# Optimization experiments

Hardware: AMD Instinct MI355X
Metric: run time of the kernel (lower is better)

Reference implementation:

```python
import jax, jax.numpy as jnp
import numpy as np

B, NPG, DEG = 512, 128, 16          # graphs, nodes/graph, out-degree
N = B * NPG                          # 65536 nodes
E = N * DEG                          # 1048576 edges
IN_DIM, HID, HEADS = 11, 32, 4
K1 = int(np.ceil(0.8 * NPG))         # 103 nodes/graph after pool1
K2 = int(np.ceil(0.8 * K1))          # 83 nodes/graph after pool2


def gat_conv(x, src, dst, mask, W, a_s, a_d, b, n_nodes):
    # PyG GATConv (concat=True, add_self_loops=True, eval mode -> no dropout)
    xp = (x @ W).reshape(n_nodes, HEADS, HID)            # [N,H,C]
    as_ = jnp.einsum('nhc,hc->nh', xp, a_s)
    ad_ = jnp.einsum('nhc,hc->nh', xp, a_d)
    loop = jnp.arange(n_nodes)
    s = jnp.concatenate([src, loop])
    d = jnp.concatenate([dst, loop])
    m = jnp.concatenate([mask, jnp.ones(n_nodes, bool)])
    logit = jax.nn.leaky_relu(as_[s] + ad_[d], 0.2)      # [E+N,H]
    logit = jnp.where(m[:, None], logit, -1e9)
    mx = jax.ops.segment_max(logit, d, num_segments=n_nodes)
    ex = jnp.exp(logit - mx[d]) * m[:, None]
    den = jax.ops.segment_sum(ex, d, num_segments=n_nodes)
    alpha = ex / (den[d] + 1e-16)                        # segment softmax over dst
    out = jax.ops.segment_sum(alpha[:, :, None] * xp[s], d, num_segments=n_nodes)
    return out.reshape(n_nodes, HEADS * HID) + b


def topk_pool(x, src, dst, mask, w, npg, k):
    # PyG TopKPooling: score = tanh((x*w).sum(-1)/||w||); keep top ceil(ratio*n) per graph
    nb = x.shape[0] // npg
    score = jnp.tanh((x @ w) / jnp.linalg.norm(w))
    vals, idx = jax.lax.top_k(score.reshape(nb, npg), k)  # [B,k]
    perm = (idx + (jnp.arange(nb) * npg)[:, None]).reshape(-1)
    x_new = x[perm] * vals.reshape(-1, 1)
    remap = jnp.full(nb * npg, -1).at[perm].set(jnp.arange(nb * k))
    ns, nd = remap[src], remap[dst]
    m = mask & (ns >= 0) & (nd >= 0)
    return x_new, jnp.where(m, ns, 0), jnp.where(m, nd, 0), m


def setup_inputs():
    key = jax.random.key(0)
    ks = jax.random.split(key, 24)
    s = 0.05
    x = jax.random.normal(ks[0], (N, IN_DIM), jnp.float32)
    src = jnp.repeat(jnp.arange(N), DEG)
    dst = (src // NPG) * NPG + jax.random.randint(ks[1], (E,), 0, NPG)
    edge_index = jnp.stack([src, dst])
    edge_attr = jax.random.normal(ks[2], (E, 4), jnp.float32)
    batch = jnp.repeat(jnp.arange(B), NPG)
    p = dict(
        W_g1=jax.random.normal(ks[3], (IN_DIM, HEADS * HID), jnp.float32) * s,
        att_src1=jax.random.normal(ks[4], (HEADS, HID), jnp.float32) * s,
        att_dst1=jax.random.normal(ks[5], (HEADS, HID), jnp.float32) * s,
        b_g1=jnp.zeros((HEADS * HID,), jnp.float32),
        W_t1=jax.random.normal(ks[6], (HEADS * HID, HID), jnp.float32) * s,
        b_t1=jnp.zeros((HID,), jnp.float32),
        pool_w1=jax.random.normal(ks[7], (HID,), jnp.float32) * s,
        W_g2=jax.random.normal(ks[8], (HID, HEADS * HID), jnp.float32) * s,
        att_src2=jax.random.normal(ks[9], (HEADS, HID), jnp.float32) * s,
        att_dst2=jax.random.normal(ks[10], (HEADS, HID), jnp.float32) * s,
        b_g2=jnp.zeros((HEADS * HID,), jnp.float32),
        W_t2=jax.random.normal(ks[11], (HEADS * HID, HID), jnp.float32) * s,
        b_t2=jnp.zeros((HID,), jnp.float32),
        pool_w2=jax.random.normal(ks[12], (HID,), jnp.float32) * s,
        W_l1=jax.random.normal(ks[13], (2 * HID, 256), jnp.float32) * s,
        b_l1=jnp.zeros((256,), jnp.float32),
        W_l2=jax.random.normal(ks[14], (256, 1024), jnp.float32) * s,
        b_l2=jnp.zeros((1024,), jnp.float32),
        W_l3=jax.random.normal(ks[15], (1024, 1), jnp.float32) * s,
        b_l3=jnp.zeros((1,), jnp.float32),
    )
    return dict(x=x, edge_index=edge_index, edge_attr=edge_attr, batch=batch, **p)


def reference(x, edge_index, edge_attr, batch,
              W_g1, att_src1, att_dst1, b_g1, W_t1, b_t1, pool_w1,
              W_g2, att_src2, att_dst2, b_g2, W_t2, b_t2, pool_w2,
              W_l1, b_l1, W_l2, b_l2, W_l3, b_l3):
    # edge_attr is ignored (GATConv built without edge_dim); batch is implicit
    # in the fixed equal-size graph layout.  Eval mode -> dropout disabled.
    src, dst = edge_index[0], edge_index[1]
    mask = jnp.ones(E, bool)
    h = jax.nn.relu(gat_conv(x, src, dst, mask, W_g1, att_src1, att_dst1, b_g1, N))
    h = h @ W_t1 + b_t1
    h, src, dst, mask = topk_pool(h, src, dst, mask, pool_w1, NPG, K1)
    h1 = h.reshape(B, K1, HID)
    g1 = jnp.concatenate([h1.max(1), h1.mean(1)], axis=1)   # [B, 2*HID]
    h = jax.nn.relu(gat_conv(h, src, dst, mask, W_g2, att_src2, att_dst2, b_g2, B * K1))
    h = h @ W_t2 + b_t2
    h, src, dst, mask = topk_pool(h, src, dst, mask, pool_w2, K1, K2)
    h2 = h.reshape(B, K2, HID)
    g2 = jnp.concatenate([h2.max(1), h2.mean(1)], axis=1)
    g = g1 + g2
    g = jax.nn.relu(g @ W_l1 + b_l1)
    g = jax.nn.relu(g @ W_l2 + b_l2)
    return g @ W_l3 + b_l3                                   # [B,1]
```

## Files before the change

kernel.cpp:

```cpp
#include <hip/hip_runtime.h>
#include <math.h>

constexpr int NPGc  = 128;
constexpr int NG    = 512;
constexpr int EPGc  = 2048;
constexpr int ETOT  = 1048576;
constexpr int IND   = 11;
constexpr int HIDc  = 32;
constexpr int FD    = 128;
constexpr int K1c   = 103;
constexpr int K2c   = 83;
constexpr int NN    = NG * NPGc;
constexpr int N2c   = NG * K1c;

__device__ __forceinline__ float lrelu(float x){ return fmaxf(x, 0.2f*x); }

template<int KIN>
__device__ void foldDev(const float* __restrict__ Wg, const float* __restrict__ avs,
                        const float* __restrict__ avd, float* __restrict__ S, float* __restrict__ D, int t)
{
    if (t < KIN * 4) {
        int k = t >> 2, h = t & 3;
        float s = 0.f, d = 0.f;
        for (int j = 0; j < HIDc; j++) {
            float w = Wg[k*FD + h*HIDc + j];
            s = fmaf(w, avs[h*HIDc + j], s);
            d = fmaf(w, avd[h*HIDc + j], d);
        }
        S[t] = s; D[t] = d;
    }
}
__global__ void k_fold2(const float* W1, const float* s1, const float* d1, float* S1, float* D1,
                        const float* W2, const float* s2, const float* d2, float* S2, float* D2)
{
    if (blockIdx.x == 0) foldDev<IND>(W1, s1, d1, S1, D1, threadIdx.x);
    else                 foldDev<HIDc>(W2, s2, d2, S2, D2, threadIdx.x);
}

template<bool REMAP>
__global__ __launch_bounds__(256) void k_csr(const int* __restrict__ ei, const int* __restrict__ rankv,
                                             int* __restrict__ csrOff, unsigned char* __restrict__ csrSB,
                                             int nnode)
{
    int g = blockIdx.x, t = threadIdx.x;
    __shared__ int cnt[128], cur[128], offL[129];
    __shared__ unsigned char sbL[EPGc];
    __shared__ signed char rmap[NPGc];
    if (t < 128) cnt[t] = 0;
    if constexpr (REMAP) { if (t < NPGc) rmap[t] = (signed char)rankv[g*NPGc + t]; }
    __syncthreads();
    const int* dstG = ei + ETOT + g * EPGc;
    int sn[8], dn[8];
    #pragma unroll
    for (int q = 0; q < 8; q++) {
        int e = t + 256*q;
        int dO = dstG[e] - g * NPGc, s0 = e >> 4;
        if constexpr (REMAP) {
            int s = rmap[s0], d = rmap[dO];
            bool ok = (s >= 0 && d >= 0);
            sn[q] = s; dn[q] = ok ? d : -1;
        } else { sn[q] = s0; dn[q] = dO; }
        if (dn[q] >= 0) atomicAdd(&cnt[dn[q]], 1);
    }
    __syncthreads();
    if (t < 64) {
        int c0 = cnt[2*t], c1 = cnt[2*t + 1], ps = c0 + c1, P = ps;
        #pragma unroll
        for (int dlt = 1; dlt < 64; dlt <<= 1) { int v = __shfl_up(P, dlt); if (t >= dlt) P += v; }
        int E0 = P - ps;
        offL[2*t] = E0; offL[2*t + 1] = E0 + c0;
        cur[2*t] = E0; cur[2*t + 1] = E0 + c0;
        if (t == 63) offL[128] = P;
    }
    __syncthreads();
    #pragma unroll
    for (int q = 0; q < 8; q++) {
        if (dn[q] >= 0) { int pos = atomicAdd(&cur[dn[q]], 1); sbL[pos] = (unsigned char)sn[q]; }
    }
    __syncthreads();
    if (t < 128) ((int4*)(csrSB + (size_t)g * EPGc))[t] = ((const int4*)sbL)[t];
    if (t <= nnode) csrOff[g*132 + t] = offL[t];
}

template<int NNODE, int KIN>
__global__ __launch_bounds__(256) void k_gat(
    const float* __restrict__ xin, const float* __restrict__ Wg,
    const float* __restrict__ WsS, const float* __restrict__ WsD,
    const int* __restrict__ csrOff, const unsigned char* __restrict__ csrSB,
    const float* __restrict__ bias, float* __restrict__ outp)
{
    int g = blockIdx.x, h = blockIdx.y, t = threadIdx.x;
    constexpr int UN = (NNODE*KIN > EPGc ? NNODE*KIN : EPGc);
    __shared__ __align__(16) float xpL[NNODE * 36];
    __shared__ __align__(16) float uni[UN];
    __shared__ __align__(16) unsigned char sbL[EPGc];
    __shared__ float asL[NNODE], adL[NNODE], mM[NNODE], sfW[NNODE], sDen[NNODE];
    __shared__ int offL[NNODE + 1];
    __shared__ float WL[KIN * 32];
    __shared__ float WsSL[KIN], WsDL[KIN], bL[32];

    float* xF  = uni;
    float* wEL = uni;

    {
        const float* xg = xin + (size_t)g * NNODE * KIN;
        if constexpr ((KIN & 3) == 0) {
            for (int i = t; i < NNODE * (KIN/4); i += 256)
                ((float4*)xF)[i] = ((const float4*)xg)[i];
        } else {
            for (int i = t; i < NNODE * KIN; i += 256) xF[i] = xg[i];
        }
    }
    for (int i = t; i < KIN * 32; i += 256) { int k = i >> 5, c = i & 31; WL[i] = Wg[k*FD + h*32 + c]; }
    if (t < KIN) { WsSL[t] = WsS[t*4 + h]; WsDL[t] = WsD[t*4 + h]; }
    if (t < 32) bL[t] = bias[h*32 + t];
    if (t <= NNODE) offL[t] = csrOff[g*132 + t];
    if (t < 128) ((int4*)sbL)[t] = ((const int4*)(csrSB + (size_t)g * EPGc))[t];
    __syncthreads();

    for (int p = t; p < NNODE * 32; p += 256) {
        int n = p >> 5, c = p & 31;
        const float* xr = xF + n * KIN;
        float acc = 0.f;
        #pragma unroll
        for (int k = 0; k < KIN; k++) acc = fmaf(xr[k], WL[k*32 + c], acc);
        xpL[n*36 + c] = acc;
    }
    if (t < NNODE) {
        const float* xr = xF + t * KIN;
        float s = 0.f, d = 0.f;
        #pragma unroll
        for (int k = 0; k < KIN; k++) { float v = xr[k]; s = fmaf(v, WsSL[k], s); d = fmaf(v, WsDL[k], d); }
        asL[t] = s; adL[t] = d;
    }
    __syncthreads();

    if (t < NNODE) {
        float as_n = asL[t], adn = adL[t];
        int lo = offL[t], hi = offL[t + 1];
        float mx = as_n;
        for (int i = lo; i < hi; i++) mx = fmaxf(mx, asL[sbL[i]]);
        float m = lrelu(mx + adn);
        float ws = expf(lrelu(as_n + adn) - m);
        float den = ws;
        for (int i = lo; i < hi; i++) {
            float w = expf(lrelu(asL[sbL[i]] + adn) - m);
            wEL[i] = w; den += w;
        }
        mM[t] = m; sfW[t] = ws; sDen[t] = den;
    }
    __syncthreads();

    const float4* X4 = (const float4*)xpL;
    for (int p = t; p < NNODE * 8; p += 256) {
        int n = p >> 3, c4 = p & 7;
        float w0 = sfW[n];
        float4 v = X4[n*9 + c4];
        float4 acc; acc.x = w0*v.x; acc.y = w0*v.y; acc.z = w0*v.z; acc.w = w0*v.w;
        int lo = offL[n], hi = offL[n + 1];
        for (int i = lo; i < hi; i++) {
            int sc = sbL[i]; float w = wEL[i];
            float4 u = X4[sc*9 + c4];
            acc.x = fmaf(w, u.x, acc.x); acc.y = fmaf(w, u.y, acc.y);
            acc.z = fmaf(w, u.z, acc.z); acc.w = fmaf(w, u.w, acc.w);
        }
        float inv = 1.f / (sDen[n] + 1e-16f);
        float4 r;
        r.x = fmaxf(fmaf(acc.x, inv, bL[c4*4 + 0]), 0.f);
        r.y = fmaxf(fmaf(acc.y, inv, bL[c4*4 + 1]), 0.f);
        r.z = fmaxf(fmaf(acc.z, inv, bL[c4*4 + 2]), 0.f);
        r.w = fmaxf(fmaf(acc.w, inv, bL[c4*4 + 3]), 0.f);
        *(float4*)(outp + (size_t)(g * NNODE + n) * FD + h*32 + c4*4) = r;
    }
}

__global__ __launch_bounds__(256) void k_lin(const float* __restrict__ in,
    const float* __restrict__ W, const float* __restrict__ b, float* __restrict__ outp)
{
    __shared__ float WtL[FD * HIDc];
    int t = threadIdx.x;
    for (int i = t; i < FD * HIDc / 4; i += 256) ((float4*)WtL)[i] = ((const float4*)W)[i];
    __syncthreads();
    int j = t & 31, rg = t >> 5;
    int r0 = blockIdx.x * 32 + rg * 4;
    const float* i0 = in + (size_t)r0 * FD;
    float bj = b[j];
    float a0 = bj, a1 = bj, a2 = bj, a3 = bj;
    for (int k4 = 0; k4 < 32; k4++) {
        float4 v0 = *(const float4*)(i0 + k4*4);
        float4 v1 = *(const float4*)(i0 + FD + k4*4);
        float4 v2 = *(const float4*)(i0 + 2*FD + k4*4);
        float4 v3 = *(const float4*)(i0 + 3*FD + k4*4);
        float w0 = WtL[(k4*4 + 0)*HIDc + j], w1 = WtL[(k4*4 + 1)*HIDc + j];
        float w2 = WtL[(k4*4 + 2)*HIDc + j], w3 = WtL[(k4*4 + 3)*HIDc + j];
        a0 = fmaf(v0.x, w0, a0); a0 = fmaf(v0.y, w1, a0); a0 = fmaf(v0.z, w2, a0); a0 = fmaf(v0.w, w3, a0);
        a1 = fmaf(v1.x, w0, a1); a1 = fmaf(v1.y, w1, a1); a1 = fmaf(v1.z, w2, a1); a1 = fmaf(v1.w, w3, a1);
        a2 = fmaf(v2.x, w0, a2); a2 = fmaf(v2.y, w1, a2); a2 = fmaf(v2.z, w2, a2); a2 = fmaf(v2.w, w3, a2);
        a3 = fmaf(v3.x, w0, a3); a3 = fmaf(v3.y, w1, a3); a3 = fmaf(v3.z, w2, a3); a3 = fmaf(v3.w, w3, a3);
    }
    size_t ob = (size_t)r0 * HIDc + j;
    outp[ob] = a0; outp[ob + 32] = a1; outp[ob + 64] = a2; outp[ob + 96] = a3;
}

template<int NIN, int KEEP, bool FIRST>
__global__ __launch_bounds__(256) void k_pool(const float* __restrict__ ht,
    const float* __restrict__ pw, float* __restrict__ xnew, int* __restrict__ rankv,
    float* __restrict__ gfeat, const float* __restrict__ gprev)
{
    int g = blockIdx.x, t = threadIdx.x;
    __shared__ float htL[NIN * 33];
    __shared__ float scoreL[NIN], valL[NIN];
    __shared__ int rnkL[NIN];
    for (int i = t; i < NIN * 8; i += 256) {
        int n = i >> 3, q = i & 7;
        float4 v = *(const float4*)(ht + (size_t)(g*NIN + n)*HIDc + q*4);
        float* dst = htL + n*33 + q*4;
        dst[0] = v.x; dst[1] = v.y; dst[2] = v.z; dst[3] = v.w;
    }
    __syncthreads();
    float nrm; { float ss = 0.f; for (int k = 0; k < HIDc; k++) { float w = pw[k]; ss = fmaf(w, w, ss); } nrm = sqrtf(ss); }
    if (t < NIN) {
        float dot = 0.f;
        for (int k = 0; k < HIDc; k++) dot = fmaf(htL[t*33 + k], pw[k], dot);
        float val = tanhf(dot / nrm);
        scoreL[t] = val; valL[t] = val;
    }
    __syncthreads();
    if (t < NIN) {
        float si = scoreL[t]; int rank = 0;
        for (int q = 0; q < NIN; q++) {
            float sj = scoreL[q];
            rank += (sj > si || (sj == si && q < t)) ? 1 : 0;
        }
        rnkL[t] = (rank < KEEP) ? rank : -1;
        if (FIRST) rankv[g*NPGc + t] = rnkL[t];
    }
    __syncthreads();
    if (FIRST) {
        for (int p = t; p < NIN * 32; p += 256) {
            int n = p >> 5, jj = p & 31;
            int rk = rnkL[n];
            if (rk >= 0) xnew[((size_t)g*KEEP + rk)*HIDc + jj] = htL[n*33 + jj] * valL[n];
        }
    }
    if (t < HIDc) {
        float mx = -INFINITY, sm = 0.f;
        for (int n = 0; n < NIN; n++) {
            if (rnkL[n] >= 0) { float v = htL[n*33 + t] * valL[n]; mx = fmaxf(mx, v); sm += v; }
        }
        float mean = sm / (float)KEEP;
        if (FIRST) {
            gfeat[(size_t)g*64 + t]      = mx;
            gfeat[(size_t)g*64 + 32 + t] = mean;
        } else {
            gfeat[(size_t)g*64 + t]      = gprev[(size_t)g*64 + t] + mx;
            gfeat[(size_t)g*64 + 32 + t] = gprev[(size_t)g*64 + 32 + t] + mean;
        }
    }
}

__global__ __launch_bounds__(256) void k_mlpA(const float* __restrict__ gsum,
    const float* __restrict__ W1, const float* __restrict__ b1,
    const float* __restrict__ W2, const float* __restrict__ b2,
    const float* __restrict__ W3, float* __restrict__ part)
{
    int gb = blockIdx.x, q = blockIdx.y, t = threadIdx.x;
    int g0 = gb * 4;
    __shared__ float gL[256];
    __shared__ float h1L[1024];
    __shared__ float4 red[256];
    gL[t] = gsum[(size_t)g0*64 + t];
    __syncthreads();
    float bv = b1[t];
    float a0 = bv, a1 = bv, a2 = bv, a3 = bv;
    #pragma unroll 4
    for (int k = 0; k < 64; k++) {
        float w = W1[k*256 + t];
        a0 = fmaf(gL[k], w, a0); a1 = fmaf(gL[64 + k], w, a1);
        a2 = fmaf(gL[128 + k], w, a2); a3 = fmaf(gL[192 + k], w, a3);
    }
    h1L[t] = fmaxf(a0, 0.f); h1L[256 + t] = fmaxf(a1, 0.f);
    h1L[512 + t] = fmaxf(a2, 0.f); h1L[768 + t] = fmaxf(a3, 0.f);
    __syncthreads();
    int o = q * 256 + t;
    float b2v = b2[o], w3 = W3[o];
    float c0 = b2v, c1 = b2v, c2 = b2v, c3 = b2v;
    const float* w2c = W2 + o;
    #pragma unroll 8
    for (int i = 0; i < 256; i++) {
        float w = w2c[(size_t)i * 1024];
        c0 = fmaf(h1L[i], w, c0); c1 = fmaf(h1L[256 + i], w, c1);
        c2 = fmaf(h1L[512 + i], w, c2); c3 = fmaf(h1L[768 + i], w, c3);
    }
    red[t] = make_float4(fmaxf(c0, 0.f)*w3, fmaxf(c1, 0.f)*w3, fmaxf(c2, 0.f)*w3, fmaxf(c3, 0.f)*w3);
    __syncthreads();
    for (int s = 128; s > 0; s >>= 1) {
        if (t < s) { float4 a = red[t], b = red[t + s]; a.x += b.x; a.y += b.y; a.z += b.z; a.w += b.w; red[t] = a; }
        __syncthreads();
    }
    if (t == 0) {
        float4 r = red[0];
        part[(size_t)(g0 + 0)*4 + q] = r.x;
        part[(size_t)(g0 + 1)*4 + q] = r.y;
        part[(size_t)(g0 + 2)*4 + q] = r.z;
        part[(size_t)(g0 + 3)*4 + q] = r.w;
    }
}

__global__ void k_mlpB(const float* __restrict__ part, const float* __restrict__ b3,
                       float* __restrict__ outp)
{
    int g = blockIdx.x * 256 + threadIdx.x;
    if (g < NG) {
        float4 p = ((const float4*)part)[g];
        outp[g] = ((p.x + p.y) + (p.z + p.w)) + b3[0];
    }
}

extern "C" void kernel_launch(void* const* d_in, const int* in_sizes, int n_in,
                              void* d_out, int out_size, void* d_ws, size_t ws_size,
                              hipStream_t stream)
{
    const float* x    = (const float*)d_in[0];
    const int*   ei   = (const int*)  d_in[1];
    const float* W_g1 = (const float*)d_in[4];
    const float* as1w = (const float*)d_in[5];
    const float* ad1w = (const float*)d_in[6];
    const float* b_g1 = (const float*)d_in[7];
    const float* W_t1 = (const float*)d_in[8];
    const float* b_t1 = (const float*)d_in[9];
    const float* pw1  = (const float*)d_in[10];
    const float* W_g2 = (const float*)d_in[11];
    const float* as2w = (const float*)d_in[12];
    const float* ad2w = (const float*)d_in[13];
    const float* b_g2 = (const float*)d_in[14];
    const float* W_t2 = (const float*)d_in[15];
    const float* b_t2 = (const float*)d_in[16];
    const float* pw2  = (const float*)d_in[17];
    const float* W_l1 = (const float*)d_in[18];
    const float* b_l1 = (const float*)d_in[19];
    const float* W_l2 = (const float*)d_in[20];
    const float* b_l2 = (const float*)d_in[21];
    const float* W_l3 = (const float*)d_in[22];
    const float* b_l3 = (const float*)d_in[23];
    float* out = (float*)d_out;

    char* ws = (char*)d_ws;
    size_t off = 0;
    auto alloc = [&](size_t bytes) -> void* {
        void* p = (void*)(ws + off);
        off += ((bytes + 255) / 256) * 256;
        return p;
    };
    float* hg1   = (float*)alloc((size_t)NN * FD * 4);
    float* ht1   = (float*)alloc((size_t)NN * HIDc * 4);
    float* x2    = (float*)alloc((size_t)N2c * HIDc * 4);
    int*   rank1 = (int*)  alloc((size_t)NN * 4);
    float* g1    = (float*)alloc((size_t)NG * 64 * 4);
    float* gsum  = (float*)alloc((size_t)NG * 64 * 4);
    float* part  = (float*)alloc((size_t)NG * 4 * 4);
    float* wsS1  = (float*)alloc(64 * 4);
    float* wsD1  = (float*)alloc(64 * 4);
    float* wsS2  = (float*)alloc(128 * 4);
    float* wsD2  = (float*)alloc(128 * 4);
    int*   off1  = (int*)  alloc((size_t)NG * 132 * 4);
    unsigned char* sb1 = (unsigned char*)alloc((size_t)NG * EPGc);
    int*   off2  = (int*)  alloc((size_t)NG * 132 * 4);
    unsigned char* sb2 = (unsigned char*)alloc((size_t)NG * EPGc);
    float* hg2 = hg1;
    float* ht2 = ht1;

    k_fold2<<<2, 128, 0, stream>>>(W_g1, as1w, ad1w, wsS1, wsD1,
                                   W_g2, as2w, ad2w, wsS2, wsD2);
    k_csr<false><<<NG, 256, 0, stream>>>(ei, nullptr, off1, sb1, NPGc);

    k_gat<NPGc, IND><<<dim3(NG, 4), 256, 0, stream>>>(
        x, W_g1, wsS1, wsD1, off1, sb1, b_g1, hg1);
    k_lin<<<NN/32, 256, 0, stream>>>(hg1, W_t1, b_t1, ht1);
    k_pool<NPGc, K1c, true><<<NG, 256, 0, stream>>>(
        ht1, pw1, x2, rank1, g1, nullptr);

    k_csr<true><<<NG, 256, 0, stream>>>(ei, rank1, off2, sb2, K1c);
    k_gat<K1c, HIDc><<<dim3(NG, 4), 256, 0, stream>>>(
        x2, W_g2, wsS2, wsD2, off2, sb2, b_g2, hg2);
    k_lin<<<N2c/32, 256, 0, stream>>>(hg2, W_t2, b_t2, ht2);
    k_pool<K1c, K2c, false><<<NG, 256, 0, stream>>>(
        ht2, pw2, nullptr, nullptr, gsum, g1);

    k_mlpA<<<dim3(NG/4, 4), 256, 0, stream>>>(gsum, W_l1, b_l1, W_l2, b_l2, W_l3, part);
    k_mlpB<<<2, 256, 0, stream>>>(part, b_l3, out);
}
```

Measured before the change: 329.4 us.

## Fuse GAT, linear transform and top-k pool into one per-graph layer kernel

Replaces the separate GAT (one block per graph per head), linear and pooling kernels with one kernel per graph that loops over the four heads and accumulates the 128->32 linear projection in registers before pooling in shared memory. This removes the global round trips of the 128-wide GAT output and the 32-wide linear output, and two launches per layer. The softmax max and exp are now edge-parallel, using a float-flip atomicMax on a new per-edge destination array produced by the CSR kernel. The trade-offs are less block parallelism (512 blocks instead of 2048 for GAT), heavy shared memory use that limits occupancy, and the heads now running one after another inside a block.

```diff
diff --git a/kernel.cpp b/kernel.cpp
--- a/kernel.cpp
+++ b/kernel.cpp
@@ -15,6 +15,15 @@
 
 __device__ __forceinline__ float lrelu(float x){ return fmaxf(x, 0.2f*x); }
 
+__device__ __forceinline__ unsigned flipF(float f){
+    unsigned u = __float_as_uint(f);
+    return u ^ (unsigned)(((int)u >> 31) | 0x80000000);
+}
+__device__ __forceinline__ float unflipF(unsigned u){
+    unsigned m = ((u >> 31) - 1u) | 0x80000000u;
+    return __uint_as_float(u ^ m);
+}
+
 template<int KIN>
 __device__ void foldDev(const float* __restrict__ Wg, const float* __restrict__ avs,
                         const float* __restrict__ avd, float* __restrict__ S, float* __restrict__ D, int t)
@@ -40,11 +49,11 @@
 template<bool REMAP>
 __global__ __launch_bounds__(256) void k_csr(const int* __restrict__ ei, const int* __restrict__ rankv,
                                              int* __restrict__ csrOff, unsigned char* __restrict__ csrSB,
-                                             int nnode)
+                                             unsigned char* __restrict__ csrDB, int nnode)
 {
     int g = blockIdx.x, t = threadIdx.x;
     __shared__ int cnt[128], cur[128], offL[129];
-    __shared__ unsigned char sbL[EPGc];
+    __shared__ unsigned char sbL[EPGc], dbL[EPGc];
     __shared__ signed char rmap[NPGc];
     if (t < 128) cnt[t] = 0;
     if constexpr (REMAP) { if (t < NPGc) rmap[t] = (signed char)rankv[g*NPGc + t]; }
@@ -75,160 +84,217 @@
     __syncthreads();
     #pragma unroll
     for (int q = 0; q < 8; q++) {
-        if (dn[q] >= 0) { int pos = atomicAdd(&cur[dn[q]], 1); sbL[pos] = (unsigned char)sn[q]; }
-    }
-    __syncthreads();
-    if (t < 128) ((int4*)(csrSB + (size_t)g * EPGc))[t] = ((const int4*)sbL)[t];
+        if (dn[q] >= 0) {
+            int pos = atomicAdd(&cur[dn[q]], 1);
+            sbL[pos] = (unsigned char)sn[q];
+            dbL[pos] = (unsigned char)dn[q];
+        }
+    }
+    __syncthreads();
+    if (t < 128) {
+        ((int4*)(csrSB + (size_t)g * EPGc))[t] = ((const int4*)sbL)[t];
+        ((int4*)(csrDB + (size_t)g * EPGc))[t] = ((const int4*)dbL)[t];
+    }
     if (t <= nnode) csrOff[g*132 + t] = offL[t];
 }
 
-template<int NNODE, int KIN>
-__global__ __launch_bounds__(256) void k_gat(
+template<int NNODE, int KIN, int KEEP, bool FIRST>
+__global__ __launch_bounds__(256, 4) void k_layer(
     const float* __restrict__ xin, const float* __restrict__ Wg,
     const float* __restrict__ WsS, const float* __restrict__ WsD,
+    const float* __restrict__ bg,
+    const float* __restrict__ Wt, const float* __restrict__ bt,
+    const float* __restrict__ pw,
     const int* __restrict__ csrOff, const unsigned char* __restrict__ csrSB,
-    const float* __restrict__ bias, float* __restrict__ outp)
-{
-    int g = blockIdx.x, h = blockIdx.y, t = threadIdx.x;
-    constexpr int UN = (NNODE*KIN > EPGc ? NNODE*KIN : EPGc);
-    __shared__ __align__(16) float xpL[NNODE * 36];
-    __shared__ __align__(16) float uni[UN];
-    __shared__ __align__(16) unsigned char sbL[EPGc];
-    __shared__ float asL[NNODE], adL[NNODE], mM[NNODE], sfW[NNODE], sDen[NNODE];
+    const unsigned char* __restrict__ csrDB,
+    float* __restrict__ xnew, int* __restrict__ rankv,
+    float* __restrict__ gfeat, const float* __restrict__ gprev)
+{
+    constexpr int NP   = (NNODE + 3) & ~3;
+    constexpr int NGRP = NP / 4;
+    int g = blockIdx.x, t = threadIdx.x;
+
+    __shared__ __align__(16) float xFT[KIN * NP];
+    __shared__ __align__(16) float WfL[KIN * FD];
+    __shared__ __align__(16) float WtL[FD * HIDc];
+    __shared__ __align__(16) float xpL[NP * 36];
+    __shared__ float wEu[EPGc];
+    __shared__ unsigned char sbL[EPGc], dbL[EPGc];
     __shared__ int offL[NNODE + 1];
-    __shared__ float WL[KIN * 32];
-    __shared__ float WsSL[KIN], WsDL[KIN], bL[32];
-
-    float* xF  = uni;
-    float* wEL = uni;
+    __shared__ float asL[NNODE], adL[NNODE], sfW[NNODE], sDi[NNODE];
+    __shared__ unsigned maxU[NNODE];
+    __shared__ __align__(8) float admL[NNODE * 2];
+    __shared__ float WsSL[KIN * 4], WsDL[KIN * 4], bgL[FD], btL[HIDc];
 
     {
         const float* xg = xin + (size_t)g * NNODE * KIN;
-        if constexpr ((KIN & 3) == 0) {
-            for (int i = t; i < NNODE * (KIN/4); i += 256)
-                ((float4*)xF)[i] = ((const float4*)xg)[i];
-        } else {
-            for (int i = t; i < NNODE * KIN; i += 256) xF[i] = xg[i];
-        }
-    }
-    for (int i = t; i < KIN * 32; i += 256) { int k = i >> 5, c = i & 31; WL[i] = Wg[k*FD + h*32 + c]; }
-    if (t < KIN) { WsSL[t] = WsS[t*4 + h]; WsDL[t] = WsD[t*4 + h]; }
-    if (t < 32) bL[t] = bias[h*32 + t];
+        for (int i = t; i < NNODE * KIN; i += 256) {
+            int n = i / KIN, k = i - n * KIN;
+            xFT[k * NP + n] = xg[i];
+        }
+        if constexpr (NP > NNODE) {
+            for (int i = t; i < KIN * (NP - NNODE); i += 256) {
+                int k = i / (NP - NNODE), n = NNODE + (i % (NP - NNODE));
+                xFT[k * NP + n] = 0.f;
+            }
+        }
+    }
+    for (int i = t; i < KIN * FD / 4; i += 256) ((float4*)WfL)[i] = ((const float4*)Wg)[i];
+    for (int i = t; i < FD * HIDc / 4; i += 256) ((float4*)WtL)[i] = ((const float4*)Wt)[i];
+    for (int i = t; i < KIN * 4; i += 256) { WsSL[i] = WsS[i]; WsDL[i] = WsD[i]; }
+    if (t < FD) bgL[t] = bg[t];
+    if (t < HIDc) btL[t] = bt[t];
     if (t <= NNODE) offL[t] = csrOff[g*132 + t];
-    if (t < 128) ((int4*)sbL)[t] = ((const int4*)(csrSB + (size_t)g * EPGc))[t];
-    __syncthreads();
-
-    for (int p = t; p < NNODE * 32; p += 256) {
-        int n = p >> 5, c = p & 31;
-        const float* xr = xF + n * KIN;
-        float acc = 0.f;
+    for (int i = t; i < EPGc / 16; i += 256) {
+        ((int4*)sbL)[i] = ((const int4*)(csrSB + (size_t)g * EPGc))[i];
+        ((int4*)dbL)[i] = ((const int4*)(csrDB + (size_t)g * EPGc))[i];
+    }
+    __syncthreads();
+    const int EC = offL[NNODE];
+
+    const int n4 = t >> 3, j4 = t & 7;
+    float4 acc0, acc1, acc2, acc3;
+    { float4 bi = make_float4(btL[j4*4], btL[j4*4+1], btL[j4*4+2], btL[j4*4+3]);
+      acc0 = bi; acc1 = bi; acc2 = bi; acc3 = bi; }
+
+    for (int h = 0; h < 4; h++) {
+        __syncthreads();
+
+        for (int id = t; id < NGRP * 32; id += 256) {
+            int grp = id >> 5, c = id & 31;
+            float4 a = make_float4(0.f, 0.f, 0.f, 0.f);
+            #pragma unroll
+            for (int k = 0; k < KIN; k++) {
+                float4 xv = *(const float4*)&xFT[k * NP + grp * 4];
+                float w = WfL[k * FD + h * 32 + c];
+                a.x = fmaf(xv.x, w, a.x); a.y = fmaf(xv.y, w, a.y);
+                a.z = fmaf(xv.z, w, a.z); a.w = fmaf(xv.w, w, a.w);
+            }
+            int nb = grp * 4;
+            xpL[(nb+0)*36 + c] = a.x; xpL[(nb+1)*36 + c] = a.y;
+            xpL[(nb+2)*36 + c] = a.z; xpL[(nb+3)*36 + c] = a.w;
+        }
+        if (t < NNODE) {
+            float s = 0.f, d = 0.f;
+            #pragma unroll
+            for (int k = 0; k < KIN; k++) {
+                float v = xFT[k * NP + t];
+                s = fmaf(v, WsSL[k*4 + h], s);
+                d = fmaf(v, WsDL[k*4 + h], d);
+            }
+            asL[t] = s; adL[t] = d; maxU[t] = flipF(s);
+        }
+        __syncthreads();
+
+        for (int s = t; s < EC; s += 256)
+            atomicMax(&maxU[dbL[s]], flipF(asL[sbL[s]]));
+        __syncthreads();
+
+        if (t < NNODE) {
+            float ad = adL[t];
+            float m = lrelu(unflipF(maxU[t]) + ad);
+            admL[2*t] = ad; admL[2*t + 1] = m;
+            sfW[t] = expf(lrelu(asL[t] + ad) - m);
+        }
+        __syncthreads();
+
+        for (int s = t; s < EC; s += 256) {
+            int sb = sbL[s], db = dbL[s];
+            float2 am = *(const float2*)&admL[2*db];
+            wEu[s] = expf(lrelu(asL[sb] + am.x) - am.y);
+        }
+        __syncthreads();
+
+        if (t < NNODE) {
+            float den = sfW[t];
+            int lo = offL[t], hi = offL[t + 1];
+            for (int s = lo; s < hi; s++) den += wEu[s];
+            sDi[t] = 1.f / (den + 1e-16f);
+        }
+        __syncthreads();
+
+        const float4* X4 = (const float4*)xpL;
+        auto aggOne = [&](int p) -> float4 {
+            int n = p >> 3, c4 = p & 7;
+            float w0 = sfW[n];
+            float4 v = X4[n*9 + c4];
+            float4 a; a.x = w0*v.x; a.y = w0*v.y; a.z = w0*v.z; a.w = w0*v.w;
+            int lo = offL[n], hi = offL[n + 1];
+            for (int s = lo; s < hi; s++) {
+                int sc = sbL[s]; float w = wEu[s];
+                float4 u = X4[sc*9 + c4];
+                a.x = fmaf(w, u.x, a.x); a.y = fmaf(w, u.y, a.y);
+                a.z = fmaf(w, u.z, a.z); a.w = fmaf(w, u.w, a.w);
+            }
+            float inv = sDi[n];
+            float4 r;
+            r.x = fmaxf(fmaf(a.x, inv, bgL[h*32 + c4*4 + 0]), 0.f);
+            r.y = fmaxf(fmaf(a.y, inv, bgL[h*32 + c4*4 + 1]), 0.f);
+            r.z = fmaxf(fmaf(a.z, inv, bgL[h*32 + c4*4 + 2]), 0.f);
+            r.w = fmaxf(fmaf(a.w, inv, bgL[h*32 + c4*4 + 3]), 0.f);
+            return r;
+        };
+        float4 rv0 = aggOne(t);
+        float4 rv1 = aggOne(t + 256);
+        float4 rv2 = aggOne(t + 512);
+        float4 rv3;
+        if (t + 768 < NNODE * 8) rv3 = aggOne(t + 768);
+        __syncthreads();
+
+        float4* X4w = (float4*)xpL;
+        X4w[(t>>3)*9 + (t&7)] = rv0;
+        { int p = t + 256; X4w[(p>>3)*9 + (p&7)] = rv1; }
+        { int p = t + 512; X4w[(p>>3)*9 + (p&7)] = rv2; }
+        if (t + 768 < NNODE * 8) { int p = t + 768; X4w[(p>>3)*9 + (p&7)] = rv3; }
+        __syncthreads();
+
+        if (n4 < NGRP) {
+            int nb = n4 * 4;
+            #pragma unroll 8
+            for (int c = 0; c < 32; c++) {
+                float4 w4 = *(const float4*)&WtL[(h*32 + c)*HIDc + j4*4];
+                float r0 = xpL[(nb+0)*36 + c], r1 = xpL[(nb+1)*36 + c];
+                float r2 = xpL[(nb+2)*36 + c], r3 = xpL[(nb+3)*36 + c];
+                acc0.x = fmaf(r0, w4.x, acc0.x); acc0.y = fmaf(r0, w4.y, acc0.y);
+                acc0.z = fmaf(r0, w4.z, acc0.z); acc0.w = fmaf(r0, w4.w, acc0.w);
+                acc1.x = fmaf(r1, w4.x, acc1.x); acc1.y = fmaf(r1, w4.y, acc1.y);
+                acc1.z = fmaf(r1, w4.z, acc1.z); acc1.w = fmaf(r1, w4.w, acc1.w);
+                acc2.x = fmaf(r2, w4.x, acc2.x); acc2.y = fmaf(r2, w4.y, acc2.y);
+                acc2.z = fmaf(r2, w4.z, acc2.z); acc2.w = fmaf(r2, w4.w, acc2.w);
+                acc3.x = fmaf(r3, w4.x, acc3.x); acc3.y = fmaf(r3, w4.y, acc3.y);
+                acc3.z = fmaf(r3, w4.z, acc3.z); acc3.w = fmaf(r3, w4.w, acc3.w);
+            }
+        }
+    }
+    __syncthreads();
+
+    float* htL = xpL;
+    if (n4 < NGRP) {
+        int nb = n4 * 4, jb = j4 * 4;
+        float4 av[4] = {acc0, acc1, acc2, acc3};
         #pragma unroll
-        for (int k = 0; k < KIN; k++) acc = fmaf(xr[k], WL[k*32 + c], acc);
-        xpL[n*36 + c] = acc;
-    }
+        for (int i = 0; i < 4; i++) {
+            int n = nb + i;
+            if (n < NNODE) {
+                htL[n*33 + jb + 0] = av[i].x; htL[n*33 + jb + 1] = av[i].y;
+                htL[n*33 + jb + 2] = av[i].z; htL[n*33 + jb + 3] = av[i].w;
+            }
+        }
+    }
+    __syncthreads();
+
+    float* scoreL = wEu;
+    int*   rnkL   = (int*)(wEu + 128);
+    float nrm; { float ss = 0.f; for (int k = 0; k < HIDc; k++) { float w = pw[k]; ss = fmaf(w, w, ss); } nrm = sqrtf(ss); }
     if (t < NNODE) {
-        const float* xr = xF + t * KIN;
-        float s = 0.f, d = 0.f;
-        #pragma unroll
-        for (int k = 0; k < KIN; k++) { float v = xr[k]; s = fmaf(v, WsSL[k], s); d = fmaf(v, WsDL[k], d); }
-        asL[t] = s; adL[t] = d;
-    }
-    __syncthreads();
-
-    if (t < NNODE) {
-        float as_n = asL[t], adn = adL[t];
-        int lo = offL[t], hi = offL[t + 1];
-        float mx = as_n;
-        for (int i = lo; i < hi; i++) mx = fmaxf(mx, asL[sbL[i]]);
-        float m = lrelu(mx + adn);
-        float ws = expf(lrelu(as_n + adn) - m);
-        float den = ws;
-        for (int i = lo; i < hi; i++) {
-            float w = expf(lrelu(asL[sbL[i]] + adn) - m);
-            wEL[i] = w; den += w;
-        }
-        mM[t] = m; sfW[t] = ws; sDen[t] = den;
-    }
-    __syncthreads();
-
-    const float4* X4 = (const float4*)xpL;
-    for (int p = t; p < NNODE * 8; p += 256) {
-        int n = p >> 3, c4 = p & 7;
-        float w0 = sfW[n];
-        float4 v = X4[n*9 + c4];
-        float4 acc; acc.x = w0*v.x; acc.y = w0*v.y; acc.z = w0*v.z; acc.w = w0*v.w;
-        int lo = offL[n], hi = offL[n + 1];
-        for (int i = lo; i < hi; i++) {
-            int sc = sbL[i]; float w = wEL[i];
-            float4 u = X4[sc*9 + c4];
-            acc.x = fmaf(w, u.x, acc.x); acc.y = fmaf(w, u.y, acc.y);
-            acc.z = fmaf(w, u.z, acc.z); acc.w = fmaf(w, u.w, acc.w);
-        }
-        float inv = 1.f / (sDen[n] + 1e-16f);
-        float4 r;
-        r.x = fmaxf(fmaf(acc.x, inv, bL[c4*4 + 0]), 0.f);
-        r.y = fmaxf(fmaf(acc.y, inv, bL[c4*4 + 1]), 0.f);
-        r.z = fmaxf(fmaf(acc.z, inv, bL[c4*4 + 2]), 0.f);
-        r.w = fmaxf(fmaf(acc.w, inv, bL[c4*4 + 3]), 0.f);
-        *(float4*)(outp + (size_t)(g * NNODE + n) * FD + h*32 + c4*4) = r;
-    }
-}
-
-__global__ __launch_bounds__(256) void k_lin(const float* __restrict__ in,
-    const float* __restrict__ W, const float* __restrict__ b, float* __restrict__ outp)
-{
-    __shared__ float WtL[FD * HIDc];
-    int t = threadIdx.x;
-    for (int i = t; i < FD * HIDc / 4; i += 256) ((float4*)WtL)[i] = ((const float4*)W)[i];
-    __syncthreads();
-    int j = t & 31, rg = t >> 5;
-    int r0 = blockIdx.x * 32 + rg * 4;
-    const float* i0 = in + (size_t)r0 * FD;
-    float bj = b[j];
-    float a0 = bj, a1 = bj, a2 = bj, a3 = bj;
-    for (int k4 = 0; k4 < 32; k4++) {
-        float4 v0 = *(const float4*)(i0 + k4*4);
-        float4 v1 = *(const float4*)(i0 + FD + k4*4);
-        float4 v2 = *(const float4*)(i0 + 2*FD + k4*4);
-        float4 v3 = *(const float4*)(i0 + 3*FD + k4*4);
-        float w0 = WtL[(k4*4 + 0)*HIDc + j], w1 = WtL[(k4*4 + 1)*HIDc + j];
-        float w2 = WtL[(k4*4 + 2)*HIDc + j], w3 = WtL[(k4*4 + 3)*HIDc + j];
-        a0 = fmaf(v0.x, w0, a0); a0 = fmaf(v0.y, w1, a0); a0 = fmaf(v0.z, w2, a0); a0 = fmaf(v0.w, w3, a0);
-        a1 = fmaf(v1.x, w0, a1); a1 = fmaf(v1.y, w1, a1); a1 = fmaf(v1.z, w2, a1); a1 = fmaf(v1.w, w3, a1);
-        a2 = fmaf(v2.x, w0, a2); a2 = fmaf(v2.y, w1, a2); a2 = fmaf(v2.z, w2, a2); a2 = fmaf(v2.w, w3, a2);
-        a3 = fmaf(v3.x, w0, a3); a3 = fmaf(v3.y, w1, a3); a3 = fmaf(v3.z, w2, a3); a3 = fmaf(v3.w, w3, a3);
-    }
-    size_t ob = (size_t)r0 * HIDc + j;
-    outp[ob] = a0; outp[ob + 32] = a1; outp[ob + 64] = a2; outp[ob + 96] = a3;
-}
-
-template<int NIN, int KEEP, bool FIRST>
-__global__ __launch_bounds__(256) void k_pool(const float* __restrict__ ht,
-    const float* __restrict__ pw, float* __restrict__ xnew, int* __restrict__ rankv,
-    float* __restrict__ gfeat, const float* __restrict__ gprev)
-{
-    int g = blockIdx.x, t = threadIdx.x;
-    __shared__ float htL[NIN * 33];
-    __shared__ float scoreL[NIN], valL[NIN];
-    __shared__ int rnkL[NIN];
-    for (int i = t; i < NIN * 8; i += 256) {
-        int n = i >> 3, q = i & 7;
-        float4 v = *(const float4*)(ht + (size_t)(g*NIN + n)*HIDc + q*4);
-        float* dst = htL + n*33 + q*4;
-        dst[0] = v.x; dst[1] = v.y; dst[2] = v.z; dst[3] = v.w;
-    }
-    __syncthreads();
-    float nrm; { float ss = 0.f; for (int k = 0; k < HIDc; k++) { float w = pw[k]; ss = fmaf(w, w, ss); } nrm = sqrtf(ss); }
-    if (t < NIN) {
         float dot = 0.f;
         for (int k = 0; k < HIDc; k++) dot = fmaf(htL[t*33 + k], pw[k], dot);
-        float val = tanhf(dot / nrm);
-        scoreL[t] = val; valL[t] = val;
-    }
-    __syncthreads();
-    if (t < NIN) {
+        scoreL[t] = tanhf(dot / nrm);
+    }
+    __syncthreads();
+    if (t < NNODE) {
         float si = scoreL[t]; int rank = 0;
-        for (int q = 0; q < NIN; q++) {
+        for (int q = 0; q < NNODE; q++) {
             float sj = scoreL[q];
             rank += (sj > si || (sj == si && q < t)) ? 1 : 0;
         }
@@ -237,16 +303,16 @@
     }
     __syncthreads();
     if (FIRST) {
-        for (int p = t; p < NIN * 32; p += 256) {
+        for (int p = t; p < NNODE * 32; p += 256) {
             int n = p >> 5, jj = p & 31;
             int rk = rnkL[n];
-            if (rk >= 0) xnew[((size_t)g*KEEP + rk)*HIDc + jj] = htL[n*33 + jj] * valL[n];
+            if (rk >= 0) xnew[((size_t)g*KEEP + rk)*HIDc + jj] = htL[n*33 + jj] * scoreL[n];
         }
     }
     if (t < HIDc) {
         float mx = -INFINITY, sm = 0.f;
-        for (int n = 0; n < NIN; n++) {
-            if (rnkL[n] >= 0) { float v = htL[n*33 + t] * valL[n]; mx = fmaxf(mx, v); sm += v; }
+        for (int n = 0; n < NNODE; n++) {
+            if (rnkL[n] >= 0) { float v = htL[n*33 + t] * scoreL[n]; mx = fmaxf(mx, v); sm += v; }
         }
         float mean = sm / (float)KEEP;
         if (FIRST) {
@@ -352,8 +418,6 @@
         off += ((bytes + 255) / 256) * 256;
         return p;
     };
-    float* hg1   = (float*)alloc((size_t)NN * FD * 4);
-    float* ht1   = (float*)alloc((size_t)NN * HIDc * 4);
     float* x2    = (float*)alloc((size_t)N2c * HIDc * 4);
     int*   rank1 = (int*)  alloc((size_t)NN * 4);
     float* g1    = (float*)alloc((size_t)NG * 64 * 4);
@@ -365,27 +429,24 @@
     float* wsD2  = (float*)alloc(128 * 4);
     int*   off1  = (int*)  alloc((size_t)NG * 132 * 4);
     unsigned char* sb1 = (unsigned char*)alloc((size_t)NG * EPGc);
+    unsigned char* db1 = (unsigned char*)alloc((size_t)NG * EPGc);
     int*   off2  = (int*)  alloc((size_t)NG * 132 * 4);
     unsigned char* sb2 = (unsigned char*)alloc((size_t)NG * EPGc);
-    float* hg2 = hg1;
-    float* ht2 = ht1;
+    unsigned char* db2 = (unsigned char*)alloc((size_t)NG * EPGc);
 
     k_fold2<<<2, 128, 0, stream>>>(W_g1, as1w, ad1w, wsS1, wsD1,
                                    W_g2, as2w, ad2w, wsS2, wsD2);
-    k_csr<false><<<NG, 256, 0, stream>>>(ei, nullptr, off1, sb1, NPGc);
-
-    k_gat<NPGc, IND><<<dim3(NG, 4), 256, 0, stream>>>(
-        x, W_g1, wsS1, wsD1, off1, sb1, b_g1, hg1);
-    k_lin<<<NN/32, 256, 0, stream>>>(hg1, W_t1, b_t1, ht1);
-    k_pool<NPGc, K1c, true><<<NG, 256, 0, stream>>>(
-        ht1, pw1, x2, rank1, g1, nullptr);
-
-    k_csr<true><<<NG, 256, 0, stream>>>(ei, rank1, off2, sb2, K1c);
-    k_gat<K1c, HIDc><<<dim3(NG, 4), 256, 0, stream>>>(
-        x2, W_g2, wsS2, wsD2, off2, sb2, b_g2, hg2);
-    k_lin<<<N2c/32, 256, 0, stream>>>(hg2, W_t2, b_t2, ht2);
-    k_pool<K1c, K2c, false><<<NG, 256, 0, stream>>>(
-        ht2, pw2, nullptr, nullptr, gsum, g1);
+    k_csr<false><<<NG, 256, 0, stream>>>(ei, nullptr, off1, sb1, db1, NPGc);
+
+    k_layer<NPGc, IND, K1c, true><<<NG, 256, 0, stream>>>(
+        x, W_g1, wsS1, wsD1, b_g1, W_t1, b_t1, pw1,
+        off1, sb1, db1, x2, rank1, g1, nullptr);
+
+    k_csr<true><<<NG, 256, 0, stream>>>(ei, rank1, off2, sb2, db2, K1c);
+
+    k_layer<K1c, HIDc, K2c, false><<<NG, 256, 0, stream>>>(
+        x2, W_g2, wsS2, wsD2, b_g2, W_t2, b_t2, pw2,
+        off2, sb2, db2, nullptr, nullptr, gsum, g1);
 
     k_mlpA<<<dim3(NG/4, 4), 256, 0, stream>>>(gsum, W_l1, b_l1, W_l2, b_l2, W_l3, part);
     k_mlpB<<<2, 256, 0, stream>>>(part, b_l3, out);
```

Result: faster. 315.2 us (-4.3%).
